# Performance work log

Hardware: AMD Instinct MI355X
Metric: run time of the kernel (lower is better)

## Reference

```python
import jax, jax.numpy as jnp
import numpy as np

N_NODES = 50000
N_EDGES = 600000
D = 128


def setup_inputs() -> dict:
    key = jax.random.key(0)
    ks = jax.random.split(key, 8)
    x = jax.random.normal(ks[0], (N_NODES, D), dtype=jnp.float32)
    edge_index = jax.random.randint(ks[1], (2, N_EDGES), 0, N_NODES, dtype=jnp.int64)
    s = 1.0 / np.sqrt(D)
    W_l1 = jax.random.uniform(ks[2], (D, D), jnp.float32, -s, s)
    W_r1 = jax.random.uniform(ks[3], (D, D), jnp.float32, -s, s)
    b1 = jnp.zeros((D,), jnp.float32)
    W_l2 = jax.random.uniform(ks[4], (D, D), jnp.float32, -s, s)
    W_r2 = jax.random.uniform(ks[5], (D, D), jnp.float32, -s, s)
    b2 = jnp.zeros((D,), jnp.float32)
    return {"x": x, "edge_index": edge_index, "W_l1": W_l1, "W_r1": W_r1,
            "b1": b1, "W_l2": W_l2, "W_r2": W_r2, "b2": b2}


def _sage_conv(x, src, dst, W_l, W_r, b):
    # mean aggregation over incoming edges (src -> dst), PyG SAGEConv semantics
    n = x.shape[0]
    msg = x[src]                                               # [E, D] gather
    agg = jax.ops.segment_sum(msg, dst, num_segments=n)        # [N, D] scatter-add
    cnt = jax.ops.segment_sum(jnp.ones((src.shape[0],), x.dtype), dst, num_segments=n)
    mean = agg / jnp.maximum(cnt, 1.0)[:, None]
    return mean @ W_l + x @ W_r + b


def reference(x, edge_index, W_l1, W_r1, b1, W_l2, W_r2, b2):
    src, dst = edge_index[0], edge_index[1]
    h = jax.nn.relu(_sage_conv(x, src, dst, W_l1, W_r1, b1))
    out = _sage_conv(h, src, dst, W_l2, W_r2, b2)
    return out
```

## Files before the change

### kernel.cpp

```cpp
#include <hip/hip_runtime.h>
#include <hip/hip_bf16.h>

#define N_NODES 50000
#define N_EDGES 600000
#define D 128
#define K2 256
#define SCAN_BLK 1024
#define NB_SCAN ((N_NODES + SCAN_BLK - 1) / SCAN_BLK)

#define CVT_BLOCKS  (N_NODES * 16 / 256)
#define HIST_BLOCKS ((N_EDGES + 255) / 256)
#define PREPW_BLOCKS (2 * D * K2 / 256)
#define PREP_GRID (CVT_BLOCKS + HIST_BLOCKS + PREPW_BLOCKS)

typedef __bf16 bf16x8 __attribute__((ext_vector_type(8)));
typedef float  f32x16 __attribute__((ext_vector_type(16)));

__device__ __forceinline__ unsigned short f32_to_bf16_rne(float f) {
    unsigned int u = __builtin_bit_cast(unsigned int, f);
    unsigned int r = (u + 0x7fffu + ((u >> 16) & 1u)) >> 16;
    return (unsigned short)r;
}
__device__ __forceinline__ unsigned pk2(float lo, float hi) {
    return (unsigned)f32_to_bf16_rne(lo) | ((unsigned)f32_to_bf16_rne(hi) << 16);
}
__device__ __forceinline__ float bfl(unsigned int u) { return __builtin_bit_cast(float, u << 16); }
__device__ __forceinline__ float bfh(unsigned int u) { return __builtin_bit_cast(float, u & 0xffff0000u); }

__global__ __launch_bounds__(256) void prep_kernel(
    const float* __restrict__ x, const int* __restrict__ ei,
    const float* __restrict__ Wl1, const float* __restrict__ Wr1,
    const float* __restrict__ Wl2, const float* __restrict__ Wr2,
    unsigned short* __restrict__ A0, unsigned short* __restrict__ WT,
    int* __restrict__ counts)
{
    const int b = blockIdx.x;
    if (b < CVT_BLOCKS) {
        int idx = b * 256 + threadIdx.x;
        int node = idx >> 4, g = idx & 15;
        const float4* xp = (const float4*)(x + (size_t)node * D + g * 8);
        float4 v0 = xp[0], v1 = xp[1];
        uint4 o;
        o.x = pk2(v0.x, v0.y); o.y = pk2(v0.z, v0.w);
        o.z = pk2(v1.x, v1.y); o.w = pk2(v1.z, v1.w);
        ((uint4*)A0)[(size_t)node * 16 + g] = o;
    } else if (b < CVT_BLOCKS + HIST_BLOCKS) {
        int e = (b - CVT_BLOCKS) * 256 + threadIdx.x;
        if (e < N_EDGES) atomicAdd(&counts[ei[N_EDGES + e]], 1);
    } else {
        int idx = (b - CVT_BLOCKS - HIST_BLOCKS) * 256 + threadIdx.x;
        int layer = idx >> 15, rem = idx & 32767;
        int n = rem >> 8, k = rem & 255;
        const float* Wl = layer ? Wl2 : Wl1;
        const float* Wr = layer ? Wr2 : Wr1;
        float v = (k < D) ? Wl[k * D + n] : Wr[(k - D) * D + n];
        WT[((size_t)layer << 15) + n * K2 + k] = f32_to_bf16_rne(v);
    }
}

__global__ __launch_bounds__(256) void scan_p1(const int* __restrict__ counts,
                                               int* __restrict__ bsum) {
    __shared__ int wsum[4];
    const int tid = threadIdx.x;
    const int lane = tid & 63, wid = tid >> 6;
    int i0 = blockIdx.x * SCAN_BLK + tid * 4;
    int t = 0;
    #pragma unroll
    for (int k = 0; k < 4; ++k) if (i0 + k < N_NODES) t += counts[i0 + k];
    int acc = t;
    #pragma unroll
    for (int d = 1; d < 64; d <<= 1) {
        int v = __shfl_up(acc, d, 64);
        if (lane >= d) acc += v;
    }
    if (lane == 63) wsum[wid] = acc;
    __syncthreads();
    if (tid == 0) bsum[blockIdx.x] = wsum[0] + wsum[1] + wsum[2] + wsum[3];
}

__global__ __launch_bounds__(256) void scan_p3(int* __restrict__ counts,
                                               const int* __restrict__ bsum,
                                               int* __restrict__ offsets) {
    __shared__ int wsum[4];
    __shared__ int bpre_s;
    const int tid = threadIdx.x;
    const int lane = tid & 63, wid = tid >> 6;
    if (tid < 64) {
        int v = (tid < blockIdx.x) ? bsum[tid] : 0;
        #pragma unroll
        for (int d = 32; d; d >>= 1) v += __shfl_xor(v, d, 64);
        if (tid == 0) bpre_s = v;
    }
    int i0 = blockIdx.x * SCAN_BLK + tid * 4;
    int c[4];
    int t = 0;
    #pragma unroll
    for (int k = 0; k < 4; ++k) {
        c[k] = (i0 + k < N_NODES) ? counts[i0 + k] : 0;
        t += c[k];
    }
    int acc = t;
    #pragma unroll
    for (int d = 1; d < 64; d <<= 1) {
        int v = __shfl_up(acc, d, 64);
        if (lane >= d) acc += v;
    }
    if (lane == 63) wsum[wid] = acc;
    __syncthreads();
    if (tid == 0) {
        int s = 0;
        #pragma unroll
        for (int w = 0; w < 4; ++w) { int v = wsum[w]; wsum[w] = s; s += v; }
    }
    __syncthreads();
    int excl = bpre_s + wsum[wid] + (acc - t);
    #pragma unroll
    for (int k = 0; k < 4; ++k) {
        if (i0 + k < N_NODES) {
            counts[i0 + k] = excl;
            offsets[i0 + k + 1] = excl + c[k];
        }
        excl += c[k];
    }
    if (blockIdx.x == 0 && tid == 0) offsets[0] = 0;
}

__global__ __launch_bounds__(256) void build_csr_kernel(const int* __restrict__ ei,
                                                        int* __restrict__ cursor,
                                                        int* __restrict__ sorted_src) {
    int e = blockIdx.x * blockDim.x + threadIdx.x;
    if (e < N_EDGES) {
        int src = ei[e];
        int dst = ei[N_EDGES + e];
        int pos = atomicAdd(&cursor[dst], 1);
        sorted_src[pos] = src;
    }
}

template <bool RELU, bool OUT_BF16>
__global__ __launch_bounds__(256) void layer_kernel(
    const unsigned short* __restrict__ Xin,
    const int* __restrict__ offsets, const int* __restrict__ srcs,
    const unsigned short* __restrict__ WT,
    const float* __restrict__ bias,
    unsigned short* __restrict__ Hout,
    float* __restrict__ outf)
{
    __shared__ uint4 As4[16 * 2 * 32];
    const int tid = threadIdx.x;
    const int base = blockIdx.x * 32;
    const uint4* X4 = (const uint4*)Xin;

    {
        const int m = tid >> 3;
        const int c = tid & 7;
        const int node = base + m;
        int beg = 0, end = 0;
        if (node < N_NODES) { beg = offsets[node]; end = offsets[node + 1]; }

        float a[16];
        #pragma unroll
        for (int k = 0; k < 16; ++k) a[k] = 0.0f;

        int e = beg;
        for (; e + 1 < end; e += 2) {
            int s0 = srcs[e], s1 = srcs[e + 1];
            uint4 v0 = X4[(size_t)s0 * 16 + c * 2];
            uint4 v1 = X4[(size_t)s0 * 16 + c * 2 + 1];
            uint4 w0 = X4[(size_t)s1 * 16 + c * 2];
            uint4 w1 = X4[(size_t)s1 * 16 + c * 2 + 1];
            a[0] += bfl(v0.x); a[1] += bfh(v0.x); a[2] += bfl(v0.y); a[3] += bfh(v0.y);
            a[4] += bfl(v0.z); a[5] += bfh(v0.z); a[6] += bfl(v0.w); a[7] += bfh(v0.w);
            a[8] += bfl(v1.x); a[9] += bfh(v1.x); a[10] += bfl(v1.y); a[11] += bfh(v1.y);
            a[12] += bfl(v1.z); a[13] += bfh(v1.z); a[14] += bfl(v1.w); a[15] += bfh(v1.w);
            a[0] += bfl(w0.x); a[1] += bfh(w0.x); a[2] += bfl(w0.y); a[3] += bfh(w0.y);
            a[4] += bfl(w0.z); a[5] += bfh(w0.z); a[6] += bfl(w0.w); a[7] += bfh(w0.w);
            a[8] += bfl(w1.x); a[9] += bfh(w1.x); a[10] += bfl(w1.y); a[11] += bfh(w1.y);
            a[12] += bfl(w1.z); a[13] += bfh(w1.z); a[14] += bfl(w1.w); a[15] += bfh(w1.w);
        }
        if (e < end) {
            int s0 = srcs[e];
            uint4 v0 = X4[(size_t)s0 * 16 + c * 2];
            uint4 v1 = X4[(size_t)s0 * 16 + c * 2 + 1];
            a[0] += bfl(v0.x); a[1] += bfh(v0.x); a[2] += bfl(v0.y); a[3] += bfh(v0.y);
            a[4] += bfl(v0.z); a[5] += bfh(v0.z); a[6] += bfl(v0.w); a[7] += bfh(v0.w);
            a[8] += bfl(v1.x); a[9] += bfh(v1.x); a[10] += bfl(v1.y); a[11] += bfh(v1.y);
            a[12] += bfl(v1.z); a[13] += bfh(v1.z); a[14] += bfl(v1.w); a[15] += bfh(v1.w);
        }
        float inv = 1.0f / fmaxf((float)(end - beg), 1.0f);
        uint4 o0, o1;
        o0.x = pk2(a[0] * inv, a[1] * inv);  o0.y = pk2(a[2] * inv, a[3] * inv);
        o0.z = pk2(a[4] * inv, a[5] * inv);  o0.w = pk2(a[6] * inv, a[7] * inv);
        o1.x = pk2(a[8] * inv, a[9] * inv);  o1.y = pk2(a[10] * inv, a[11] * inv);
        o1.z = pk2(a[12] * inv, a[13] * inv); o1.w = pk2(a[14] * inv, a[15] * inv);
        As4[(c * 2 + 0) * 32 + m] = o0;
        As4[(c * 2 + 1) * 32 + m] = o1;
        uint4 x0 = {0, 0, 0, 0}, x1 = {0, 0, 0, 0};
        if (node < N_NODES) {
            x0 = X4[(size_t)node * 16 + c * 2];
            x1 = X4[(size_t)node * 16 + c * 2 + 1];
        }
        As4[((8 + c) * 2 + 0) * 32 + m] = x0;
        As4[((8 + c) * 2 + 1) * 32 + m] = x1;
    }
    __syncthreads();

    const int l = tid & 63;
    const int w = tid >> 6;
    const int m = l & 31;
    const int kg = l >> 5;
    const int col = w * 32 + m;
    const uint4* bp = (const uint4*)(WT + (size_t)col * K2 + kg * 8);
    const bf16x8* afrag = (const bf16x8*)As4;

    f32x16 acc = {};
    #pragma unroll
    for (int s = 0; s < 16; ++s) {
        bf16x8 a = afrag[(s * 2 + kg) * 32 + m];
        bf16x8 b = __builtin_bit_cast(bf16x8, bp[s * 2]);
        acc = __builtin_amdgcn_mfma_f32_32x32x16_bf16(a, b, acc, 0, 0, 0);
    }

    const float bc = bias[col];
    const int halfadd = kg * 4;
    #pragma unroll
    for (int r = 0; r < 16; ++r) {
        int rw = base + (r & 3) + 8 * (r >> 2) + halfadd;
        if (rw < N_NODES) {
            float v = acc[r] + bc;
            if (RELU) v = fmaxf(v, 0.0f);
            if (OUT_BF16) Hout[(size_t)rw * D + col] = f32_to_bf16_rne(v);
            else outf[(size_t)rw * D + col] = v;
        }
    }
}

extern "C" void kernel_launch(void* const* d_in, const int* in_sizes, int n_in,
                              void* d_out, int out_size, void* d_ws, size_t ws_size,
                              hipStream_t stream) {
    const float* x   = (const float*)d_in[0];
    const int*   ei  = (const int*)d_in[1];
    const float* Wl1 = (const float*)d_in[2];
    const float* Wr1 = (const float*)d_in[3];
    const float* b1  = (const float*)d_in[4];
    const float* Wl2 = (const float*)d_in[5];
    const float* Wr2 = (const float*)d_in[6];
    const float* b2  = (const float*)d_in[7];
    float* out = (float*)d_out;

    unsigned short* A0 = (unsigned short*)d_ws;
    unsigned short* A1 = A0 + (size_t)N_NODES * D;
    unsigned short* WT = A1 + (size_t)N_NODES * D;
    int* counts  = (int*)(WT + 2 * D * K2);
    int* offsets = counts + N_NODES;
    int* srcs    = offsets + N_NODES + 1;
    int* bsum    = srcs + N_EDGES;

    const int layerBlocks = (N_NODES + 31) / 32;

    hipMemsetAsync(counts, 0, N_NODES * sizeof(int), stream);
    prep_kernel<<<PREP_GRID, 256, 0, stream>>>(x, ei, Wl1, Wr1, Wl2, Wr2, A0, WT, counts);
    scan_p1<<<NB_SCAN, 256, 0, stream>>>(counts, bsum);
    scan_p3<<<NB_SCAN, 256, 0, stream>>>(counts, bsum, offsets);
    build_csr_kernel<<<HIST_BLOCKS, 256, 0, stream>>>(ei, counts, srcs);

    layer_kernel<true, true><<<layerBlocks, 256, 0, stream>>>(
        A0, offsets, srcs, WT, b1, A1, nullptr);
    layer_kernel<false, false><<<layerBlocks, 256, 0, stream>>>(
        A1, offsets, srcs, WT + (size_t)D * K2, b2, nullptr, out);
}
```

Baseline: 224.1 us.

## Fuse all stages into one cooperative persistent kernel with grid syncs

```diff
diff --git a/kernel.cpp b/kernel.cpp
--- a/kernel.cpp
+++ b/kernel.cpp
@@ -1,5 +1,7 @@
 #include <hip/hip_runtime.h>
 #include <hip/hip_bf16.h>
+#include <hip/hip_cooperative_groups.h>
+namespace cg = cooperative_groups;
 
 #define N_NODES 50000
 #define N_EDGES 600000
@@ -7,11 +9,8 @@
 #define K2 256
 #define SCAN_BLK 1024
 #define NB_SCAN ((N_NODES + SCAN_BLK - 1) / SCAN_BLK)
-
-#define CVT_BLOCKS  (N_NODES * 16 / 256)
-#define HIST_BLOCKS ((N_EDGES + 255) / 256)
-#define PREPW_BLOCKS (2 * D * K2 / 256)
-#define PREP_GRID (CVT_BLOCKS + HIST_BLOCKS + PREPW_BLOCKS)
+#define NB_MEGA 782
+#define N_TILES ((N_NODES + 31) / 32)
 
 typedef __bf16 bf16x8 __attribute__((ext_vector_type(8)));
 typedef float  f32x16 __attribute__((ext_vector_type(16)));
@@ -27,16 +26,14 @@
 __device__ __forceinline__ float bfl(unsigned int u) { return __builtin_bit_cast(float, u << 16); }
 __device__ __forceinline__ float bfh(unsigned int u) { return __builtin_bit_cast(float, u & 0xffff0000u); }
 
-__global__ __launch_bounds__(256) void prep_kernel(
-    const float* __restrict__ x, const int* __restrict__ ei,
-    const float* __restrict__ Wl1, const float* __restrict__ Wr1,
-    const float* __restrict__ Wl2, const float* __restrict__ Wr2,
-    unsigned short* __restrict__ A0, unsigned short* __restrict__ WT,
-    int* __restrict__ counts)
-{
-    const int b = blockIdx.x;
-    if (b < CVT_BLOCKS) {
-        int idx = b * 256 + threadIdx.x;
+
+__device__ __forceinline__ void do_zero(int* counts, int g0, int gs) {
+    for (int i = g0; i < N_NODES; i += gs) counts[i] = 0;
+}
+
+__device__ __forceinline__ void do_cvt(const float* __restrict__ x,
+                                       unsigned short* __restrict__ A0, int g0, int gs) {
+    for (int idx = g0; idx < N_NODES * 16; idx += gs) {
         int node = idx >> 4, g = idx & 15;
         const float4* xp = (const float4*)(x + (size_t)node * D + g * 8);
         float4 v0 = xp[0], v1 = xp[1];
@@ -44,11 +41,13 @@
         o.x = pk2(v0.x, v0.y); o.y = pk2(v0.z, v0.w);
         o.z = pk2(v1.x, v1.y); o.w = pk2(v1.z, v1.w);
         ((uint4*)A0)[(size_t)node * 16 + g] = o;
-    } else if (b < CVT_BLOCKS + HIST_BLOCKS) {
-        int e = (b - CVT_BLOCKS) * 256 + threadIdx.x;
-        if (e < N_EDGES) atomicAdd(&counts[ei[N_EDGES + e]], 1);
-    } else {
-        int idx = (b - CVT_BLOCKS - HIST_BLOCKS) * 256 + threadIdx.x;
+    }
+}
+
+__device__ __forceinline__ void do_prepw(const float* __restrict__ Wl1, const float* __restrict__ Wr1,
+                                         const float* __restrict__ Wl2, const float* __restrict__ Wr2,
+                                         unsigned short* __restrict__ WT, int g0, int gs) {
+    for (int idx = g0; idx < 65536; idx += gs) {
         int layer = idx >> 15, rem = idx & 32767;
         int n = rem >> 8, k = rem & 255;
         const float* Wl = layer ? Wl2 : Wl1;
@@ -58,12 +57,25 @@
     }
 }
 
-__global__ __launch_bounds__(256) void scan_p1(const int* __restrict__ counts,
-                                               int* __restrict__ bsum) {
-    __shared__ int wsum[4];
+__device__ __forceinline__ void do_hist(const int* __restrict__ ei, int* counts, int g0, int gs) {
+    for (int e = g0; e < N_EDGES; e += gs) atomicAdd(&counts[ei[N_EDGES + e]], 1);
+}
+
+__device__ __forceinline__ void do_csr(const int* __restrict__ ei, int* cursor,
+                                       int* __restrict__ srcs, int g0, int gs) {
+    for (int e = g0; e < N_EDGES; e += gs) {
+        int src = ei[e];
+        int dst = ei[N_EDGES + e];
+        int pos = atomicAdd(&cursor[dst], 1);
+        srcs[pos] = src;
+    }
+}
+
+__device__ __forceinline__ void do_scansum(const int* __restrict__ counts,
+                                           int* __restrict__ bsum, int bid, int* wsum) {
     const int tid = threadIdx.x;
     const int lane = tid & 63, wid = tid >> 6;
-    int i0 = blockIdx.x * SCAN_BLK + tid * 4;
+    int i0 = bid * SCAN_BLK + tid * 4;
     int t = 0;
     #pragma unroll
     for (int k = 0; k < 4; ++k) if (i0 + k < N_NODES) t += counts[i0 + k];
@@ -75,23 +87,23 @@
     }
     if (lane == 63) wsum[wid] = acc;
     __syncthreads();
-    if (tid == 0) bsum[blockIdx.x] = wsum[0] + wsum[1] + wsum[2] + wsum[3];
-}
-
-__global__ __launch_bounds__(256) void scan_p3(int* __restrict__ counts,
-                                               const int* __restrict__ bsum,
-                                               int* __restrict__ offsets) {
-    __shared__ int wsum[4];
-    __shared__ int bpre_s;
+    if (tid == 0) bsum[bid] = wsum[0] + wsum[1] + wsum[2] + wsum[3];
+    __syncthreads();
+}
+
+__device__ __forceinline__ void do_scanwrite(int* __restrict__ counts,
+                                             const int* __restrict__ bsum,
+                                             int* __restrict__ offsets, int bid,
+                                             int* wsum, int* bpre_s) {
     const int tid = threadIdx.x;
     const int lane = tid & 63, wid = tid >> 6;
     if (tid < 64) {
-        int v = (tid < blockIdx.x) ? bsum[tid] : 0;
+        int v = (tid < bid) ? bsum[tid] : 0;
         #pragma unroll
         for (int d = 32; d; d >>= 1) v += __shfl_xor(v, d, 64);
-        if (tid == 0) bpre_s = v;
-    }
-    int i0 = blockIdx.x * SCAN_BLK + tid * 4;
+        if (tid == 0) *bpre_s = v;
+    }
+    int i0 = bid * SCAN_BLK + tid * 4;
     int c[4];
     int t = 0;
     #pragma unroll
@@ -113,7 +125,7 @@
         for (int w = 0; w < 4; ++w) { int v = wsum[w]; wsum[w] = s; s += v; }
     }
     __syncthreads();
-    int excl = bpre_s + wsum[wid] + (acc - t);
+    int excl = *bpre_s + wsum[wid] + (acc - t);
     #pragma unroll
     for (int k = 0; k < 4; ++k) {
         if (i0 + k < N_NODES) {
@@ -122,117 +134,184 @@
         }
         excl += c[k];
     }
-    if (blockIdx.x == 0 && tid == 0) offsets[0] = 0;
-}
-
-__global__ __launch_bounds__(256) void build_csr_kernel(const int* __restrict__ ei,
-                                                        int* __restrict__ cursor,
-                                                        int* __restrict__ sorted_src) {
-    int e = blockIdx.x * blockDim.x + threadIdx.x;
-    if (e < N_EDGES) {
-        int src = ei[e];
-        int dst = ei[N_EDGES + e];
-        int pos = atomicAdd(&cursor[dst], 1);
-        sorted_src[pos] = src;
-    }
-}
-
+    if (bid == 0 && tid == 0) offsets[0] = 0;
+    __syncthreads();
+}
+
+template <bool RELU, bool OUT_BF16>
+__device__ __forceinline__ void layer_phase(uint4* As4,
+    const unsigned short* __restrict__ Xin, const int* __restrict__ offsets,
+    const int* __restrict__ srcs, const unsigned short* __restrict__ WT,
+    const float* __restrict__ bias, unsigned short* __restrict__ Hout,
+    float* __restrict__ outf, int bid, int nblocks)
+{
+    const int tid = threadIdx.x;
+    const uint4* X4 = (const uint4*)Xin;
+
+    for (int tile = bid; tile < N_TILES; tile += nblocks) {
+        const int base = tile * 32;
+        __syncthreads();
+
+        {
+            const int m = tid >> 3;
+            const int c = tid & 7;
+            const int node = base + m;
+            int beg = 0, end = 0;
+            if (node < N_NODES) { beg = offsets[node]; end = offsets[node + 1]; }
+
+            float a[16];
+            #pragma unroll
+            for (int k = 0; k < 16; ++k) a[k] = 0.0f;
+
+            int e = beg;
+            for (; e + 1 < end; e += 2) {
+                int s0 = srcs[e], s1 = srcs[e + 1];
+                uint4 v0 = X4[(size_t)s0 * 16 + c * 2];
+                uint4 v1 = X4[(size_t)s0 * 16 + c * 2 + 1];
+                uint4 w0 = X4[(size_t)s1 * 16 + c * 2];
+                uint4 w1 = X4[(size_t)s1 * 16 + c * 2 + 1];
+                a[0] += bfl(v0.x); a[1] += bfh(v0.x); a[2] += bfl(v0.y); a[3] += bfh(v0.y);
+                a[4] += bfl(v0.z); a[5] += bfh(v0.z); a[6] += bfl(v0.w); a[7] += bfh(v0.w);
+                a[8] += bfl(v1.x); a[9] += bfh(v1.x); a[10] += bfl(v1.y); a[11] += bfh(v1.y);
+                a[12] += bfl(v1.z); a[13] += bfh(v1.z); a[14] += bfl(v1.w); a[15] += bfh(v1.w);
+                a[0] += bfl(w0.x); a[1] += bfh(w0.x); a[2] += bfl(w0.y); a[3] += bfh(w0.y);
+                a[4] += bfl(w0.z); a[5] += bfh(w0.z); a[6] += bfl(w0.w); a[7] += bfh(w0.w);
+                a[8] += bfl(w1.x); a[9] += bfh(w1.x); a[10] += bfl(w1.y); a[11] += bfh(w1.y);
+                a[12] += bfl(w1.z); a[13] += bfh(w1.z); a[14] += bfl(w1.w); a[15] += bfh(w1.w);
+            }
+            if (e < end) {
+                int s0 = srcs[e];
+                uint4 v0 = X4[(size_t)s0 * 16 + c * 2];
+                uint4 v1 = X4[(size_t)s0 * 16 + c * 2 + 1];
+                a[0] += bfl(v0.x); a[1] += bfh(v0.x); a[2] += bfl(v0.y); a[3] += bfh(v0.y);
+                a[4] += bfl(v0.z); a[5] += bfh(v0.z); a[6] += bfl(v0.w); a[7] += bfh(v0.w);
+                a[8] += bfl(v1.x); a[9] += bfh(v1.x); a[10] += bfl(v1.y); a[11] += bfh(v1.y);
+                a[12] += bfl(v1.z); a[13] += bfh(v1.z); a[14] += bfl(v1.w); a[15] += bfh(v1.w);
+            }
+            float inv = 1.0f / fmaxf((float)(end - beg), 1.0f);
+            uint4 o0, o1;
+            o0.x = pk2(a[0] * inv, a[1] * inv);   o0.y = pk2(a[2] * inv, a[3] * inv);
+            o0.z = pk2(a[4] * inv, a[5] * inv);   o0.w = pk2(a[6] * inv, a[7] * inv);
+            o1.x = pk2(a[8] * inv, a[9] * inv);   o1.y = pk2(a[10] * inv, a[11] * inv);
+            o1.z = pk2(a[12] * inv, a[13] * inv); o1.w = pk2(a[14] * inv, a[15] * inv);
+            As4[(c * 2 + 0) * 32 + m] = o0;
+            As4[(c * 2 + 1) * 32 + m] = o1;
+            uint4 x0 = {0, 0, 0, 0}, x1 = {0, 0, 0, 0};
+            if (node < N_NODES) {
+                x0 = X4[(size_t)node * 16 + c * 2];
+                x1 = X4[(size_t)node * 16 + c * 2 + 1];
+            }
+            As4[((8 + c) * 2 + 0) * 32 + m] = x0;
+            As4[((8 + c) * 2 + 1) * 32 + m] = x1;
+        }
+        __syncthreads();
+
+        {
+            const int l = tid & 63;
+            const int w = tid >> 6;
+            const int m = l & 31;
+            const int kg = l >> 5;
+            const int col = w * 32 + m;
+            const uint4* bp = (const uint4*)(WT + (size_t)col * K2 + kg * 8);
+            const bf16x8* afrag = (const bf16x8*)As4;
+
+            f32x16 acc = {};
+            #pragma unroll
+            for (int s = 0; s < 16; ++s) {
+                bf16x8 a = afrag[(s * 2 + kg) * 32 + m];
+                bf16x8 b = __builtin_bit_cast(bf16x8, bp[s * 2]);
+                acc = __builtin_amdgcn_mfma_f32_32x32x16_bf16(a, b, acc, 0, 0, 0);
+            }
+
+            const float bc = bias[col];
+            const int halfadd = kg * 4;
+            #pragma unroll
+            for (int r = 0; r < 16; ++r) {
+                int rw = base + (r & 3) + 8 * (r >> 2) + halfadd;
+                if (rw < N_NODES) {
+                    float v = acc[r] + bc;
+                    if (RELU) v = fmaxf(v, 0.0f);
+                    if (OUT_BF16) Hout[(size_t)rw * D + col] = f32_to_bf16_rne(v);
+                    else outf[(size_t)rw * D + col] = v;
+                }
+            }
+        }
+    }
+}
+
+__global__ __launch_bounds__(256, 4) void mega_kernel(
+    const float* __restrict__ x, const int* __restrict__ ei,
+    const float* __restrict__ Wl1, const float* __restrict__ Wr1, const float* __restrict__ b1,
+    const float* __restrict__ Wl2, const float* __restrict__ Wr2, const float* __restrict__ b2,
+    unsigned short* A0, unsigned short* A1, unsigned short* WT,
+    int* counts, int* offsets, int* srcs, int* bsum, float* out)
+{
+    cg::grid_group grid = cg::this_grid();
+    __shared__ uint4 As4[16 * 2 * 32];
+    __shared__ int wsum[4];
+    __shared__ int bpre_s;
+
+    const int bid = blockIdx.x;
+    const int g0 = bid * 256 + threadIdx.x;
+    const int gs = gridDim.x * 256;
+
+    do_zero(counts, g0, gs);
+    do_cvt(x, A0, g0, gs);
+    do_prepw(Wl1, Wr1, Wl2, Wr2, WT, g0, gs);
+    grid.sync();
+
+    do_hist(ei, counts, g0, gs);
+    grid.sync();
+
+    if (bid < NB_SCAN) do_scansum(counts, bsum, bid, wsum);
+    grid.sync();
+
+    if (bid < NB_SCAN) do_scanwrite(counts, bsum, offsets, bid, wsum, &bpre_s);
+    grid.sync();
+
+    do_csr(ei, counts, srcs, g0, gs);
+    grid.sync();
+
+    layer_phase<true, true>(As4, A0, offsets, srcs, WT, b1, A1, nullptr, bid, gridDim.x);
+    grid.sync();
+
+    layer_phase<false, false>(As4, A1, offsets, srcs, WT + (size_t)D * K2, b2, nullptr, out, bid, gridDim.x);
+}
+
+__global__ __launch_bounds__(256) void prep_kernel(
+    const float* __restrict__ x,
+    const float* __restrict__ Wl1, const float* __restrict__ Wr1,
+    const float* __restrict__ Wl2, const float* __restrict__ Wr2,
+    unsigned short* A0, unsigned short* WT, int* counts) {
+    const int g0 = blockIdx.x * 256 + threadIdx.x;
+    const int gs = gridDim.x * 256;
+    do_zero(counts, g0, gs);
+    do_cvt(x, A0, g0, gs);
+    do_prepw(Wl1, Wr1, Wl2, Wr2, WT, g0, gs);
+}
+__global__ __launch_bounds__(256) void hist_kernel(const int* __restrict__ ei, int* counts) {
+    do_hist(ei, counts, blockIdx.x * 256 + threadIdx.x, gridDim.x * 256);
+}
+__global__ __launch_bounds__(256) void scan_s1(const int* __restrict__ counts, int* bsum) {
+    __shared__ int wsum[4];
+    do_scansum(counts, bsum, blockIdx.x, wsum);
+}
+__global__ __launch_bounds__(256) void scan_s3(int* counts, const int* bsum, int* offsets) {
+    __shared__ int wsum[4];
+    __shared__ int bpre_s;
+    do_scanwrite(counts, bsum, offsets, blockIdx.x, wsum, &bpre_s);
+}
+__global__ __launch_bounds__(256) void csr_kernel(const int* __restrict__ ei, int* cursor, int* srcs) {
+    do_csr(ei, cursor, srcs, blockIdx.x * 256 + threadIdx.x, gridDim.x * 256);
+}
 template <bool RELU, bool OUT_BF16>
 __global__ __launch_bounds__(256) void layer_kernel(
-    const unsigned short* __restrict__ Xin,
-    const int* __restrict__ offsets, const int* __restrict__ srcs,
-    const unsigned short* __restrict__ WT,
-    const float* __restrict__ bias,
-    unsigned short* __restrict__ Hout,
-    float* __restrict__ outf)
-{
+    const unsigned short* __restrict__ Xin, const int* __restrict__ offsets,
+    const int* __restrict__ srcs, const unsigned short* __restrict__ WT,
+    const float* __restrict__ bias, unsigned short* Hout, float* outf) {
     __shared__ uint4 As4[16 * 2 * 32];
-    const int tid = threadIdx.x;
-    const int base = blockIdx.x * 32;
-    const uint4* X4 = (const uint4*)Xin;
-
-    {
-        const int m = tid >> 3;
-        const int c = tid & 7;
-        const int node = base + m;
-        int beg = 0, end = 0;
-        if (node < N_NODES) { beg = offsets[node]; end = offsets[node + 1]; }
-
-        float a[16];
-        #pragma unroll
-        for (int k = 0; k < 16; ++k) a[k] = 0.0f;
-
-        int e = beg;
-        for (; e + 1 < end; e += 2) {
-            int s0 = srcs[e], s1 = srcs[e + 1];
-            uint4 v0 = X4[(size_t)s0 * 16 + c * 2];
-            uint4 v1 = X4[(size_t)s0 * 16 + c * 2 + 1];
-            uint4 w0 = X4[(size_t)s1 * 16 + c * 2];
-            uint4 w1 = X4[(size_t)s1 * 16 + c * 2 + 1];
-            a[0] += bfl(v0.x); a[1] += bfh(v0.x); a[2] += bfl(v0.y); a[3] += bfh(v0.y);
-            a[4] += bfl(v0.z); a[5] += bfh(v0.z); a[6] += bfl(v0.w); a[7] += bfh(v0.w);
-            a[8] += bfl(v1.x); a[9] += bfh(v1.x); a[10] += bfl(v1.y); a[11] += bfh(v1.y);
-            a[12] += bfl(v1.z); a[13] += bfh(v1.z); a[14] += bfl(v1.w); a[15] += bfh(v1.w);
-            a[0] += bfl(w0.x); a[1] += bfh(w0.x); a[2] += bfl(w0.y); a[3] += bfh(w0.y);
-            a[4] += bfl(w0.z); a[5] += bfh(w0.z); a[6] += bfl(w0.w); a[7] += bfh(w0.w);
-            a[8] += bfl(w1.x); a[9] += bfh(w1.x); a[10] += bfl(w1.y); a[11] += bfh(w1.y);
-            a[12] += bfl(w1.z); a[13] += bfh(w1.z); a[14] += bfl(w1.w); a[15] += bfh(w1.w);
-        }
-        if (e < end) {
-            int s0 = srcs[e];
-            uint4 v0 = X4[(size_t)s0 * 16 + c * 2];
-            uint4 v1 = X4[(size_t)s0 * 16 + c * 2 + 1];
-            a[0] += bfl(v0.x); a[1] += bfh(v0.x); a[2] += bfl(v0.y); a[3] += bfh(v0.y);
-            a[4] += bfl(v0.z); a[5] += bfh(v0.z); a[6] += bfl(v0.w); a[7] += bfh(v0.w);
-            a[8] += bfl(v1.x); a[9] += bfh(v1.x); a[10] += bfl(v1.y); a[11] += bfh(v1.y);
-            a[12] += bfl(v1.z); a[13] += bfh(v1.z); a[14] += bfl(v1.w); a[15] += bfh(v1.w);
-        }
-        float inv = 1.0f / fmaxf((float)(end - beg), 1.0f);
-        uint4 o0, o1;
-        o0.x = pk2(a[0] * inv, a[1] * inv);  o0.y = pk2(a[2] * inv, a[3] * inv);
-        o0.z = pk2(a[4] * inv, a[5] * inv);  o0.w = pk2(a[6] * inv, a[7] * inv);
-        o1.x = pk2(a[8] * inv, a[9] * inv);  o1.y = pk2(a[10] * inv, a[11] * inv);
-        o1.z = pk2(a[12] * inv, a[13] * inv); o1.w = pk2(a[14] * inv, a[15] * inv);
-        As4[(c * 2 + 0) * 32 + m] = o0;
-        As4[(c * 2 + 1) * 32 + m] = o1;
-        uint4 x0 = {0, 0, 0, 0}, x1 = {0, 0, 0, 0};
-        if (node < N_NODES) {
-            x0 = X4[(size_t)node * 16 + c * 2];
-            x1 = X4[(size_t)node * 16 + c * 2 + 1];
-        }
-        As4[((8 + c) * 2 + 0) * 32 + m] = x0;
-        As4[((8 + c) * 2 + 1) * 32 + m] = x1;
-    }
-    __syncthreads();
-
-    const int l = tid & 63;
-    const int w = tid >> 6;
-    const int m = l & 31;
-    const int kg = l >> 5;
-    const int col = w * 32 + m;
-    const uint4* bp = (const uint4*)(WT + (size_t)col * K2 + kg * 8);
-    const bf16x8* afrag = (const bf16x8*)As4;
-
-    f32x16 acc = {};
-    #pragma unroll
-    for (int s = 0; s < 16; ++s) {
-        bf16x8 a = afrag[(s * 2 + kg) * 32 + m];
-        bf16x8 b = __builtin_bit_cast(bf16x8, bp[s * 2]);
-        acc = __builtin_amdgcn_mfma_f32_32x32x16_bf16(a, b, acc, 0, 0, 0);
-    }
-
-    const float bc = bias[col];
-    const int halfadd = kg * 4;
-    #pragma unroll
-    for (int r = 0; r < 16; ++r) {
-        int rw = base + (r & 3) + 8 * (r >> 2) + halfadd;
-        if (rw < N_NODES) {
-            float v = acc[r] + bc;
-            if (RELU) v = fmaxf(v, 0.0f);
-            if (OUT_BF16) Hout[(size_t)rw * D + col] = f32_to_bf16_rne(v);
-            else outf[(size_t)rw * D + col] = v;
-        }
-    }
+    layer_phase<RELU, OUT_BF16>(As4, Xin, offsets, srcs, WT, bias, Hout, outf,
+                                blockIdx.x, gridDim.x);
 }
 
 extern "C" void kernel_launch(void* const* d_in, const int* in_sizes, int n_in,
@@ -256,16 +335,20 @@
     int* srcs    = offsets + N_NODES + 1;
     int* bsum    = srcs + N_EDGES;
 
-    const int layerBlocks = (N_NODES + 31) / 32;
-
-    hipMemsetAsync(counts, 0, N_NODES * sizeof(int), stream);
-    prep_kernel<<<PREP_GRID, 256, 0, stream>>>(x, ei, Wl1, Wr1, Wl2, Wr2, A0, WT, counts);
-    scan_p1<<<NB_SCAN, 256, 0, stream>>>(counts, bsum);
-    scan_p3<<<NB_SCAN, 256, 0, stream>>>(counts, bsum, offsets);
-    build_csr_kernel<<<HIST_BLOCKS, 256, 0, stream>>>(ei, counts, srcs);
-
-    layer_kernel<true, true><<<layerBlocks, 256, 0, stream>>>(
-        A0, offsets, srcs, WT, b1, A1, nullptr);
-    layer_kernel<false, false><<<layerBlocks, 256, 0, stream>>>(
-        A1, offsets, srcs, WT + (size_t)D * K2, b2, nullptr, out);
-}
+    void* args[] = {(void*)&x, (void*)&ei, (void*)&Wl1, (void*)&Wr1, (void*)&b1,
+                    (void*)&Wl2, (void*)&Wr2, (void*)&b2,
+                    (void*)&A0, (void*)&A1, (void*)&WT,
+                    (void*)&counts, (void*)&offsets, (void*)&srcs, (void*)&bsum, (void*)&out};
+    hipError_t err = hipLaunchCooperativeKernel((void*)mega_kernel, dim3(NB_MEGA), dim3(256),
+                                                args, 0, stream);
+    if (err != hipSuccess) {
+        prep_kernel<<<1024, 256, 0, stream>>>(x, Wl1, Wr1, Wl2, Wr2, A0, WT, counts);
+        hist_kernel<<<1024, 256, 0, stream>>>(ei, counts);
+        scan_s1<<<NB_SCAN, 256, 0, stream>>>(counts, bsum);
+        scan_s3<<<NB_SCAN, 256, 0, stream>>>(counts, bsum, offsets);
+        csr_kernel<<<1024, 256, 0, stream>>>(ei, counts, srcs);
+        layer_kernel<true, true><<<N_TILES, 256, 0, stream>>>(A0, offsets, srcs, WT, b1, A1, nullptr);
+        layer_kernel<false, false><<<N_TILES, 256, 0, stream>>>(A1, offsets, srcs,
+                                                                WT + (size_t)D * K2, b2, nullptr, out);
+    }
+}
```

New measurement: 779.7 us. 248% more time.
